# Performance work log

Hardware: AMD Instinct MI355X
Metric: run time of the kernel (lower is better)

## Reference

```python
import jax, jax.numpy as jnp
import numpy as np

TWO_PI = 2.0 * np.pi
EPS = 1e-12  # torch F.normalize eps


def setup_inputs() -> dict:
    key = jax.random.key(0)
    ks = jax.random.split(key, 12)
    B, NS, G = 16, 128, 20000
    P, S, E, T = 200, 128, 128, 50
    return {
        "x_genes": jax.random.normal(ks[0], (B, NS, G), jnp.float32),
        "tissue_idx": jax.random.randint(ks[1], (B, NS), 0, T, jnp.int32),
        "pathway_idx": jax.random.randint(ks[2], (P, S), 0, G, jnp.int32),
        "W_proj": jax.random.normal(ks[3], (P, E, S), jnp.float32) * (1.0 / np.sqrt(S)),
        "b_proj": jax.random.normal(ks[4], (P, E), jnp.float32) * 0.02,
        "tissue_table": jax.random.normal(ks[5], (T, E), jnp.float32),
        "W1": jax.random.normal(ks[6], (E, 32), jnp.float32) * (1.0 / np.sqrt(E)),
        "b1": jax.random.normal(ks[7], (32,), jnp.float32) * 0.02,
        "W2": jax.random.normal(ks[8], (32, 2), jnp.float32) * (1.0 / np.sqrt(32)),
        "b2": jax.random.normal(ks[9], (2,), jnp.float32) * 0.02,
        "Wdec": jax.random.normal(ks[10], (2, G), jnp.float32) * (1.0 / np.sqrt(2.0)),
        "bdec": jax.random.normal(ks[11], (G,), jnp.float32) * 0.02,
    }


def _l2norm(v):
    n = jnp.sqrt(jnp.sum(v * v, axis=-1, keepdims=True))
    return v / jnp.maximum(n, EPS)


def reference(x_genes, tissue_idx, pathway_idx, W_proj, b_proj, tissue_table,
              W1, b1, W2, b2, Wdec, bdec):
    B, NS, G = x_genes.shape
    x = x_genes.reshape(-1, G)            # [N, G], N = B*NS
    t = tissue_idx.reshape(-1)            # [N]

    # Pathway tokenizer: gather gene subsets + per-pathway linear (grouped GEMM)
    xg = x[:, pathway_idx]                # [N, P, S]
    H = jax.nn.relu(jnp.einsum('nps,pes->npe', xg, W_proj) + b_proj)  # [N, P, E]

    # Single-query attention with tissue embedding as query
    Q = tissue_table[t]                   # [N, E]
    scale = 1.0 / np.sqrt(H.shape[-1])
    scores = jnp.einsum('ne,npe->np', Q, H) * scale   # [N, P]
    attn = jax.nn.softmax(scores, axis=-1)
    context = jnp.einsum('np,npe->ne', attn, H)       # [N, E]

    # to_latent MLP (dropout=0 / eval)
    h = jax.nn.relu(context @ W1 + b1)
    pc = h @ W2 + b2                      # [N, 2]
    pcn = _l2norm(pc)
    ang = jnp.remainder(jnp.arctan2(pcn[:, 1], pcn[:, 0]) + TWO_PI, TWO_PI)

    # decode + normalize
    rec = _l2norm(pcn @ Wdec + bdec)      # [N, G]

    return (pcn.reshape(B, NS, 2), ang.reshape(B, NS), rec.reshape(B, NS, G))
```

## Files before the change

### kernel.cpp

```cpp
#include <hip/hip_runtime.h>
#include <cmath>

#define GG 20000
#define NN 2048
#define PP 200
#define SS 128
#define EE 128
#define TN 128
#define TPP 4
#define NSPLIT 50

typedef __bf16 bf16x8 __attribute__((ext_vector_type(8)));
typedef float f32x16 __attribute__((ext_vector_type(16)));
typedef unsigned short u16x8 __attribute__((ext_vector_type(8)));

__device__ __align__(16) unsigned g_xTi[(size_t)GG * NN];
__device__ __align__(16) unsigned short g_Wsw[(size_t)PP * 2 * 16384];
__device__ float g_ctx[(size_t)NN * NSPLIT * EE];
__device__ float g_m[NN * NSPLIT];
__device__ float g_l[NN * NSPLIT];
__device__ float g_pcn[NN * 2];

__device__ __forceinline__ unsigned short f2bf(float f) {
  unsigned u = __builtin_bit_cast(unsigned, f);
  return (unsigned short)((u + 0x7FFFu + ((u >> 16) & 1u)) >> 16);
}
__device__ __forceinline__ float bf2f(unsigned short h) {
  return __builtin_bit_cast(float, (unsigned)h << 16);
}
__device__ __forceinline__ unsigned packhl(float f) {
  unsigned short h = f2bf(f);
  unsigned short l = f2bf(f - bf2f(h));
  return (unsigned)h | ((unsigned)l << 16);
}

__global__ __launch_bounds__(256) void transpose_convert_kernel(
    const float* __restrict__ x)
{
  __shared__ float tile[64][65];
  const int g0 = blockIdx.x * 64;
  const int n0 = blockIdx.y * 64;
  const int t = threadIdx.x;
  {
    const int gq = t & 15, nl4 = t >> 4;
    #pragma unroll
    for (int k = 0; k < 4; ++k) {
      int nl = nl4 + 16 * k;
      int g = g0 + gq * 4;
      if (g + 3 < GG) {
        float4 v = *(const float4*)&x[(size_t)(n0 + nl) * GG + g];
        tile[gq * 4 + 0][nl] = v.x;
        tile[gq * 4 + 1][nl] = v.y;
        tile[gq * 4 + 2][nl] = v.z;
        tile[gq * 4 + 3][nl] = v.w;
      }
    }
  }
  __syncthreads();
  {
    const int nq = t & 15, gl4 = t >> 4;
    #pragma unroll
    for (int k = 0; k < 4; ++k) {
      int gl = gl4 + 16 * k;
      int g = g0 + gl;
      if (g < GG) {
        uint4 v;
        v.x = packhl(tile[gl][nq * 4 + 0]);
        v.y = packhl(tile[gl][nq * 4 + 1]);
        v.z = packhl(tile[gl][nq * 4 + 2]);
        v.w = packhl(tile[gl][nq * 4 + 3]);
        *(uint4*)&g_xTi[(size_t)g * NN + n0 + nq * 4] = v;
      }
    }
  }
}

__global__ __launch_bounds__(256) void wconvert_kernel(const float* __restrict__ Wp)
{
  unsigned v = blockIdx.x * 256 + threadIdx.x;
  const int si = v & 7;
  const int slp = (v >> 3) & 7;
  const int e = (v >> 6) & 127;
  const int ch = (v >> 13) & 1;
  const int p = v >> 14;
  const int slot = slp ^ (e & 7);
  const int s = ch * 64 + slot * 8 + si;
  float f = Wp[((size_t)p * EE + e) * SS + s];
  unsigned short h = f2bf(f);
  unsigned short l = f2bf(f - bf2f(h));
  size_t base = (size_t)(p * 2 + ch) * 16384 + e * 64 + slp * 8 + si;
  g_Wsw[base] = h;
  g_Wsw[base + 8192] = l;
}

__device__ __forceinline__ void stage_w(int p, int ch, unsigned short* ldsbase,
                                        int w, int ln) {
  const unsigned short* src = g_Wsw + (size_t)(p * 2 + ch) * 16384 + w * 4096 + ln * 8;
  unsigned short* ld = ldsbase + w * 4096;
  #pragma unroll
  for (int j = 0; j < 8; ++j) {
    __builtin_amdgcn_global_load_lds(
        (const __attribute__((address_space(1))) unsigned int*)(src + j * 512),
        (__attribute__((address_space(3))) unsigned int*)(ld + j * 512), 16, 0, 0);
  }
}

__device__ __forceinline__ void load_x(const int* __restrict__ pidx, int p, int ch,
                                       int kh, int ncol, unsigned* xr) {
  const int* pg = pidx + p * SS + ch * 64 + kh * 8;
  #pragma unroll
  for (int ks = 0; ks < 4; ++ks)
    #pragma unroll
    for (int j = 0; j < 8; ++j) {
      int g = pg[ks * 16 + j];
      xr[ks * 8 + j] = g_xTi[(size_t)g * NN + ncol];
    }
}

__device__ __forceinline__ void compute_chunk(const unsigned short* wb,
                                              const unsigned* xr, f32x16* acc,
                                              int nl, int kh) {
  const unsigned short* wAh = wb;
  const unsigned short* wAl = wb + 8192;
  #pragma unroll
  for (int ks = 0; ks < 4; ++ks) {
    u16x8 bhu, blu;
    #pragma unroll
    for (int j = 0; j < 8; ++j) {
      unsigned v = xr[ks * 8 + j];
      bhu[j] = (unsigned short)(v & 0xffffu);
      blu[j] = (unsigned short)(v >> 16);
    }
    bf16x8 bh = __builtin_bit_cast(bf16x8, bhu);
    bf16x8 bl = __builtin_bit_cast(bf16x8, blu);
    #pragma unroll
    for (int et = 0; et < 4; ++et) {
      const int e = et * 32 + nl;
      const int slp = (ks * 2 + kh) ^ (e & 7);
      bf16x8 ah = __builtin_bit_cast(bf16x8, *(const uint4*)(wAh + e * 64 + slp * 8));
      bf16x8 al = __builtin_bit_cast(bf16x8, *(const uint4*)(wAl + e * 64 + slp * 8));
      acc[et] = __builtin_amdgcn_mfma_f32_32x32x16_bf16(ah, bh, acc[et], 0, 0, 0);
      acc[et] = __builtin_amdgcn_mfma_f32_32x32x16_bf16(ah, bl, acc[et], 0, 0, 0);
      acc[et] = __builtin_amdgcn_mfma_f32_32x32x16_bf16(al, bh, acc[et], 0, 0, 0);
    }
  }
}

__global__ __launch_bounds__(256, 2) void proj_mfma_kernel(
    const int* __restrict__ tidx, const int* __restrict__ pidx,
    const float* __restrict__ bp, const float* __restrict__ tt)
{
  __shared__ __align__(16) unsigned short wbuf[2][16384];

  const int t = threadIdx.x;
  const int w = t >> 6;
  const int ln = t & 63;
  const int nl = ln & 31;
  const int kh = ln >> 5;
  const int n0 = blockIdx.x * TN;
  const int split = blockIdx.y;
  const int ncol = n0 + w * 32 + nl;
  const int tid_n = tidx[ncol];

  f32x16 ctx[4];
  #pragma unroll
  for (int et = 0; et < 4; ++et)
    #pragma unroll
    for (int r = 0; r < 16; ++r) ctx[et][r] = 0.f;
  float m_r = -1e30f, l_r = 0.f;

  unsigned xA[32], xB[32];

  {
    const int p = split * TPP;
    stage_w(p, 0, wbuf[0], w, ln);
    load_x(pidx, p, 0, kh, ncol, xA);
  }
  __syncthreads();

  for (int pp = 0; pp < TPP; ++pp) {
    const int p = split * TPP + pp;
    f32x16 acc[4];
    #pragma unroll
    for (int et = 0; et < 4; ++et)
      #pragma unroll
      for (int r = 0; r < 16; ++r) acc[et][r] = 0.f;

    stage_w(p, 1, wbuf[1], w, ln);
    load_x(pidx, p, 1, kh, ncol, xB);
    compute_chunk(wbuf[0], xA, acc, nl, kh);
    __syncthreads();

    if (pp + 1 < TPP) {
      stage_w(p + 1, 0, wbuf[0], w, ln);
      load_x(pidx, p + 1, 0, kh, ncol, xA);
    }
    compute_chunk(wbuf[1], xB, acc, nl, kh);

    const float4* qp = (const float4*)(tt + (size_t)tid_n * EE);
    const float4* bpv = (const float4*)(bp + (size_t)p * EE);
    float scr = 0.f;
    #pragma unroll
    for (int et = 0; et < 4; ++et)
      #pragma unroll
      for (int rq = 0; rq < 4; ++rq) {
        int e4 = (et * 32 + rq * 8 + kh * 4) >> 2;
        float4 q4 = qp[e4];
        float4 b4 = bpv[e4];
        float h0 = fmaxf(acc[et][rq * 4 + 0] + b4.x, 0.f);
        float h1 = fmaxf(acc[et][rq * 4 + 1] + b4.y, 0.f);
        float h2 = fmaxf(acc[et][rq * 4 + 2] + b4.z, 0.f);
        float h3 = fmaxf(acc[et][rq * 4 + 3] + b4.w, 0.f);
        acc[et][rq * 4 + 0] = h0; acc[et][rq * 4 + 1] = h1;
        acc[et][rq * 4 + 2] = h2; acc[et][rq * 4 + 3] = h3;
        scr += h0 * q4.x + h1 * q4.y + h2 * q4.z + h3 * q4.w;
      }
    scr += __shfl_xor(scr, 32);
    const float s_r = scr * 0.08838834764831845f;
    const float mn = fmaxf(m_r, s_r);
    const float f = expf(m_r - mn);
    const float wg = expf(s_r - mn);
    l_r = l_r * f + wg;
    m_r = mn;
    #pragma unroll
    for (int et = 0; et < 4; ++et)
      #pragma unroll
      for (int r = 0; r < 16; ++r)
        ctx[et][r] = ctx[et][r] * f + wg * acc[et][r];

    __syncthreads();
  }

  float* tbuf = (float*)wbuf;
  float* tb = tbuf + w * (32 * 128);
  #pragma unroll
  for (int et = 0; et < 4; ++et)
    #pragma unroll
    for (int rq = 0; rq < 4; ++rq) {
      int slot = et * 8 + rq * 2 + kh;
      float4 v = make_float4(ctx[et][rq * 4 + 0], ctx[et][rq * 4 + 1],
                             ctx[et][rq * 4 + 2], ctx[et][rq * 4 + 3]);
      *(float4*)&tb[nl * 128 + ((slot ^ nl) << 2)] = v;
    }
  __syncthreads();
  {
    const int rrow = ln >> 1, eh = (ln & 1) * 16;
    const int nn = n0 + w * 32 + rrow;
    float* dst = g_ctx + ((size_t)nn * NSPLIT + split) * EE + eh * 4;
    const float* srcrow = tb + rrow * 128;
    #pragma unroll
    for (int k = 0; k < 16; ++k) {
      int slot = eh + k;
      *(float4*)&dst[k * 4] = *(const float4*)&srcrow[(slot ^ rrow) << 2];
    }
  }
  if (ln < 32) {
    g_m[(size_t)ncol * NSPLIT + split] = m_r;
    g_l[(size_t)ncol * NSPLIT + split] = l_r;
  }
}

__global__ __launch_bounds__(128) void combine_kernel(
    const float* __restrict__ W1, const float* __restrict__ b1,
    const float* __restrict__ W2, const float* __restrict__ b2,
    float* __restrict__ out)
{
  const int n = blockIdx.x;
  const int t = threadIdx.x;
  __shared__ float sm[NSPLIT], slv[NSPLIT], ws[NSPLIT], ctxs[EE], hsh[32];

  if (t < NSPLIT) sm[t] = g_m[(size_t)n * NSPLIT + t];
  else if (t < 2 * NSPLIT) slv[t - NSPLIT] = g_l[(size_t)n * NSPLIT + t - NSPLIT];
  __syncthreads();
  if (t < NSPLIT) {
    float M = -1e30f;
    for (int s = 0; s < NSPLIT; ++s) M = fmaxf(M, sm[s]);
    ws[t] = expf(sm[t] - M);
  }
  __syncthreads();
  float L = 0.f;
  for (int s = 0; s < NSPLIT; ++s) L += slv[s] * ws[s];
  float c = 0.f;
  for (int s = 0; s < NSPLIT; ++s)
    c += ws[s] * g_ctx[((size_t)n * NSPLIT + s) * EE + t];
  ctxs[t] = c / L;
  __syncthreads();
  if (t < 32) {
    float h = b1[t];
    for (int e = 0; e < EE; ++e) h += ctxs[e] * W1[e * 32 + t];
    hsh[t] = fmaxf(h, 0.f);
  }
  __syncthreads();
  if (t == 0) {
    float p0 = b2[0], p1 = b2[1];
    #pragma unroll
    for (int k = 0; k < 32; ++k) { p0 += hsh[k] * W2[k * 2]; p1 += hsh[k] * W2[k * 2 + 1]; }
    float inv = 1.f / fmaxf(sqrtf(p0 * p0 + p1 * p1), 1e-12f);
    float q0 = p0 * inv, q1 = p1 * inv;
    const float PI2 = 6.2831853071795864769f;
    float ang = atan2f(q1, q0) + PI2;
    if (ang >= PI2) ang -= PI2;
    out[n * 2 + 0] = q0;
    out[n * 2 + 1] = q1;
    out[2 * NN + n] = ang;
    g_pcn[n * 2 + 0] = q0;
    g_pcn[n * 2 + 1] = q1;
  }
}

__global__ __launch_bounds__(256) void rec_kernel(
    const float* __restrict__ Wdec, const float* __restrict__ bdec,
    float* __restrict__ out)
{
  const int n = blockIdx.x;
  const int t = threadIdx.x;
  __shared__ float red[4];

  const float q0 = g_pcn[n * 2 + 0];
  const float q1 = g_pcn[n * 2 + 1];

  float ss = 0.f;
  for (int i = t; i < GG / 4; i += 256) {
    float4 w0 = *(const float4*)&Wdec[i * 4];
    float4 w1 = *(const float4*)&Wdec[GG + i * 4];
    float4 bd = *(const float4*)&bdec[i * 4];
    float v0 = q0 * w0.x + q1 * w1.x + bd.x;
    float v1 = q0 * w0.y + q1 * w1.y + bd.y;
    float v2 = q0 * w0.z + q1 * w1.z + bd.z;
    float v3 = q0 * w0.w + q1 * w1.w + bd.w;
    ss += v0 * v0 + v1 * v1 + v2 * v2 + v3 * v3;
  }
  #pragma unroll
  for (int off = 32; off >= 1; off >>= 1) ss += __shfl_xor(ss, off);
  if ((t & 63) == 0) red[t >> 6] = ss;
  __syncthreads();
  const float inv = 1.f / fmaxf(sqrtf(red[0] + red[1] + red[2] + red[3]), 1e-12f);

  float* orec = out + 3 * NN + (size_t)n * GG;
  for (int i = t; i < GG / 4; i += 256) {
    float4 w0 = *(const float4*)&Wdec[i * 4];
    float4 w1 = *(const float4*)&Wdec[GG + i * 4];
    float4 bd = *(const float4*)&bdec[i * 4];
    float4 o;
    o.x = (q0 * w0.x + q1 * w1.x + bd.x) * inv;
    o.y = (q0 * w0.y + q1 * w1.y + bd.y) * inv;
    o.z = (q0 * w0.z + q1 * w1.z + bd.z) * inv;
    o.w = (q0 * w0.w + q1 * w1.w + bd.w) * inv;
    *(float4*)&orec[i * 4] = o;
  }
}

extern "C" void kernel_launch(void* const* d_in, const int* in_sizes, int n_in,
                              void* d_out, int out_size, void* d_ws, size_t ws_size,
                              hipStream_t stream) {
  (void)in_sizes; (void)n_in; (void)out_size; (void)d_ws; (void)ws_size;
  const float* x    = (const float*)d_in[0];
  const int*   tidx = (const int*)  d_in[1];
  const int*   pidx = (const int*)  d_in[2];
  const float* Wp   = (const float*)d_in[3];
  const float* bp   = (const float*)d_in[4];
  const float* tt   = (const float*)d_in[5];
  const float* W1   = (const float*)d_in[6];
  const float* b1   = (const float*)d_in[7];
  const float* W2   = (const float*)d_in[8];
  const float* b2   = (const float*)d_in[9];
  const float* Wdec = (const float*)d_in[10];
  const float* bdec = (const float*)d_in[11];
  float* out = (float*)d_out;

  dim3 gridT((GG + 63) / 64, NN / 64, 1);
  transpose_convert_kernel<<<gridT, 256, 0, stream>>>(x);
  wconvert_kernel<<<(PP * 16384) / 256, 256, 0, stream>>>(Wp);

  dim3 gridA(NN / TN, NSPLIT, 1);
  proj_mfma_kernel<<<gridA, 256, 0, stream>>>(tidx, pidx, bp, tt);

  combine_kernel<<<NN, 128, 0, stream>>>(W1, b1, W2, b2, out);
  rec_kernel<<<NN, 256, 0, stream>>>(Wdec, bdec, out);
}
```

Before: 348.0 us.

## Assign one pathway per block and move the softmax reduction into combine

The projection kernel drops the per-block loop over 4 pathways and its double-buffered online softmax. Each block now handles a single pathway: it loads that pathway's full weights into LDS at once and writes the raw score and ReLU output per pathway. The combine kernel then computes the softmax over all 200 pathway scores with warp reductions and takes the weighted sum of the contexts using 256 threads. This creates more blocks and shorter dependency chains, but the per-pathway context buffer grows fourfold, so global write and read traffic rises sharply, and load/compute overlap is lost.

```diff
diff --git a/kernel.cpp b/kernel.cpp
--- a/kernel.cpp
+++ b/kernel.cpp
@@ -7,18 +7,16 @@
 #define SS 128
 #define EE 128
 #define TN 128
-#define TPP 4
-#define NSPLIT 50
+#define NSPLIT 200
 
 typedef __bf16 bf16x8 __attribute__((ext_vector_type(8)));
 typedef float f32x16 __attribute__((ext_vector_type(16)));
 typedef unsigned short u16x8 __attribute__((ext_vector_type(8)));
 
 __device__ __align__(16) unsigned g_xTi[(size_t)GG * NN];
-__device__ __align__(16) unsigned short g_Wsw[(size_t)PP * 2 * 16384];
+__device__ __align__(16) unsigned short g_Wsw[(size_t)PP * 32768];
 __device__ float g_ctx[(size_t)NN * NSPLIT * EE];
 __device__ float g_m[NN * NSPLIT];
-__device__ float g_l[NN * NSPLIT];
 __device__ float g_pcn[NN * 2];
 
 __device__ __forceinline__ unsigned short f2bf(float f) {
@@ -93,64 +91,13 @@
   g_Wsw[base + 8192] = l;
 }
 
-__device__ __forceinline__ void stage_w(int p, int ch, unsigned short* ldsbase,
-                                        int w, int ln) {
-  const unsigned short* src = g_Wsw + (size_t)(p * 2 + ch) * 16384 + w * 4096 + ln * 8;
-  unsigned short* ld = ldsbase + w * 4096;
-  #pragma unroll
-  for (int j = 0; j < 8; ++j) {
-    __builtin_amdgcn_global_load_lds(
-        (const __attribute__((address_space(1))) unsigned int*)(src + j * 512),
-        (__attribute__((address_space(3))) unsigned int*)(ld + j * 512), 16, 0, 0);
-  }
-}
-
-__device__ __forceinline__ void load_x(const int* __restrict__ pidx, int p, int ch,
-                                       int kh, int ncol, unsigned* xr) {
-  const int* pg = pidx + p * SS + ch * 64 + kh * 8;
-  #pragma unroll
-  for (int ks = 0; ks < 4; ++ks)
-    #pragma unroll
-    for (int j = 0; j < 8; ++j) {
-      int g = pg[ks * 16 + j];
-      xr[ks * 8 + j] = g_xTi[(size_t)g * NN + ncol];
-    }
-}
-
-__device__ __forceinline__ void compute_chunk(const unsigned short* wb,
-                                              const unsigned* xr, f32x16* acc,
-                                              int nl, int kh) {
-  const unsigned short* wAh = wb;
-  const unsigned short* wAl = wb + 8192;
-  #pragma unroll
-  for (int ks = 0; ks < 4; ++ks) {
-    u16x8 bhu, blu;
-    #pragma unroll
-    for (int j = 0; j < 8; ++j) {
-      unsigned v = xr[ks * 8 + j];
-      bhu[j] = (unsigned short)(v & 0xffffu);
-      blu[j] = (unsigned short)(v >> 16);
-    }
-    bf16x8 bh = __builtin_bit_cast(bf16x8, bhu);
-    bf16x8 bl = __builtin_bit_cast(bf16x8, blu);
-    #pragma unroll
-    for (int et = 0; et < 4; ++et) {
-      const int e = et * 32 + nl;
-      const int slp = (ks * 2 + kh) ^ (e & 7);
-      bf16x8 ah = __builtin_bit_cast(bf16x8, *(const uint4*)(wAh + e * 64 + slp * 8));
-      bf16x8 al = __builtin_bit_cast(bf16x8, *(const uint4*)(wAl + e * 64 + slp * 8));
-      acc[et] = __builtin_amdgcn_mfma_f32_32x32x16_bf16(ah, bh, acc[et], 0, 0, 0);
-      acc[et] = __builtin_amdgcn_mfma_f32_32x32x16_bf16(ah, bl, acc[et], 0, 0, 0);
-      acc[et] = __builtin_amdgcn_mfma_f32_32x32x16_bf16(al, bh, acc[et], 0, 0, 0);
-    }
-  }
-}
-
 __global__ __launch_bounds__(256, 2) void proj_mfma_kernel(
     const int* __restrict__ tidx, const int* __restrict__ pidx,
     const float* __restrict__ bp, const float* __restrict__ tt)
 {
-  __shared__ __align__(16) unsigned short wbuf[2][16384];
+  __shared__ __align__(16) unsigned short wbuf[32768];
+  __shared__ int sidx[SS];
+  __shared__ float sbp[EE];
 
   const int t = threadIdx.x;
   const int w = t >> 6;
@@ -158,95 +105,104 @@
   const int nl = ln & 31;
   const int kh = ln >> 5;
   const int n0 = blockIdx.x * TN;
-  const int split = blockIdx.y;
+  const int p = blockIdx.y;
   const int ncol = n0 + w * 32 + nl;
   const int tid_n = tidx[ncol];
 
-  f32x16 ctx[4];
+  if (t < 128) sidx[t] = pidx[p * SS + t];
+  else         sbp[t - 128] = bp[p * EE + (t - 128)];
+  __syncthreads();
+
+  {
+    const unsigned short* src = g_Wsw + (size_t)p * 32768 + w * 512 + ln * 8;
+    unsigned short* dst = wbuf + w * 512;
+    #pragma unroll
+    for (int j = 0; j < 16; ++j) {
+      __builtin_amdgcn_global_load_lds(
+          (const __attribute__((address_space(1))) unsigned int*)(src + j * 2048),
+          (__attribute__((address_space(3))) unsigned int*)(dst + j * 2048), 16, 0, 0);
+    }
+  }
+
+  unsigned xr[64];
+  #pragma unroll
+  for (int ks = 0; ks < 8; ++ks)
+    #pragma unroll
+    for (int j = 0; j < 8; ++j) {
+      int s = ks * 16 + kh * 8 + j;
+      int g = sidx[s];
+      xr[ks * 8 + j] = g_xTi[(size_t)g * NN + ncol];
+    }
+  __syncthreads();
+
+  f32x16 acc[4];
   #pragma unroll
   for (int et = 0; et < 4; ++et)
     #pragma unroll
-    for (int r = 0; r < 16; ++r) ctx[et][r] = 0.f;
-  float m_r = -1e30f, l_r = 0.f;
-
-  unsigned xA[32], xB[32];
-
-  {
-    const int p = split * TPP;
-    stage_w(p, 0, wbuf[0], w, ln);
-    load_x(pidx, p, 0, kh, ncol, xA);
-  }
-  __syncthreads();
-
-  for (int pp = 0; pp < TPP; ++pp) {
-    const int p = split * TPP + pp;
-    f32x16 acc[4];
-    #pragma unroll
-    for (int et = 0; et < 4; ++et)
-      #pragma unroll
-      for (int r = 0; r < 16; ++r) acc[et][r] = 0.f;
-
-    stage_w(p, 1, wbuf[1], w, ln);
-    load_x(pidx, p, 1, kh, ncol, xB);
-    compute_chunk(wbuf[0], xA, acc, nl, kh);
-    __syncthreads();
-
-    if (pp + 1 < TPP) {
-      stage_w(p + 1, 0, wbuf[0], w, ln);
-      load_x(pidx, p + 1, 0, kh, ncol, xA);
-    }
-    compute_chunk(wbuf[1], xB, acc, nl, kh);
-
-    const float4* qp = (const float4*)(tt + (size_t)tid_n * EE);
-    const float4* bpv = (const float4*)(bp + (size_t)p * EE);
-    float scr = 0.f;
-    #pragma unroll
-    for (int et = 0; et < 4; ++et)
-      #pragma unroll
-      for (int rq = 0; rq < 4; ++rq) {
-        int e4 = (et * 32 + rq * 8 + kh * 4) >> 2;
-        float4 q4 = qp[e4];
-        float4 b4 = bpv[e4];
-        float h0 = fmaxf(acc[et][rq * 4 + 0] + b4.x, 0.f);
-        float h1 = fmaxf(acc[et][rq * 4 + 1] + b4.y, 0.f);
-        float h2 = fmaxf(acc[et][rq * 4 + 2] + b4.z, 0.f);
-        float h3 = fmaxf(acc[et][rq * 4 + 3] + b4.w, 0.f);
-        acc[et][rq * 4 + 0] = h0; acc[et][rq * 4 + 1] = h1;
-        acc[et][rq * 4 + 2] = h2; acc[et][rq * 4 + 3] = h3;
-        scr += h0 * q4.x + h1 * q4.y + h2 * q4.z + h3 * q4.w;
-      }
-    scr += __shfl_xor(scr, 32);
-    const float s_r = scr * 0.08838834764831845f;
-    const float mn = fmaxf(m_r, s_r);
-    const float f = expf(m_r - mn);
-    const float wg = expf(s_r - mn);
-    l_r = l_r * f + wg;
-    m_r = mn;
-    #pragma unroll
-    for (int et = 0; et < 4; ++et)
-      #pragma unroll
-      for (int r = 0; r < 16; ++r)
-        ctx[et][r] = ctx[et][r] * f + wg * acc[et][r];
-
-    __syncthreads();
-  }
-
-  float* tbuf = (float*)wbuf;
-  float* tb = tbuf + w * (32 * 128);
+    for (int r = 0; r < 16; ++r) acc[et][r] = 0.f;
+
+  #pragma unroll
+  for (int ks = 0; ks < 8; ++ks) {
+    const unsigned short* wAh = wbuf + (ks >> 2) * 16384;
+    const unsigned short* wAl = wAh + 8192;
+    const int ksl = ks & 3;
+    u16x8 bhu, blu;
+    #pragma unroll
+    for (int j = 0; j < 8; ++j) {
+      unsigned v = xr[ks * 8 + j];
+      bhu[j] = (unsigned short)(v & 0xffffu);
+      blu[j] = (unsigned short)(v >> 16);
+    }
+    bf16x8 bh = __builtin_bit_cast(bf16x8, bhu);
+    bf16x8 bl = __builtin_bit_cast(bf16x8, blu);
+    #pragma unroll
+    for (int et = 0; et < 4; ++et) {
+      const int e = et * 32 + nl;
+      const int slp = (ksl * 2 + kh) ^ (e & 7);
+      bf16x8 ah = __builtin_bit_cast(bf16x8, *(const uint4*)(wAh + e * 64 + slp * 8));
+      bf16x8 al = __builtin_bit_cast(bf16x8, *(const uint4*)(wAl + e * 64 + slp * 8));
+      acc[et] = __builtin_amdgcn_mfma_f32_32x32x16_bf16(ah, bh, acc[et], 0, 0, 0);
+      acc[et] = __builtin_amdgcn_mfma_f32_32x32x16_bf16(ah, bl, acc[et], 0, 0, 0);
+      acc[et] = __builtin_amdgcn_mfma_f32_32x32x16_bf16(al, bh, acc[et], 0, 0, 0);
+    }
+  }
+
+  const float4* qp = (const float4*)(tt + (size_t)tid_n * EE);
+  float scr = 0.f;
+  #pragma unroll
+  for (int et = 0; et < 4; ++et)
+    #pragma unroll
+    for (int rq = 0; rq < 4; ++rq) {
+      int e4 = (et * 32 + rq * 8 + kh * 4) >> 2;
+      float4 q4 = qp[e4];
+      float4 b4 = *(const float4*)&sbp[e4 * 4];
+      float h0 = fmaxf(acc[et][rq * 4 + 0] + b4.x, 0.f);
+      float h1 = fmaxf(acc[et][rq * 4 + 1] + b4.y, 0.f);
+      float h2 = fmaxf(acc[et][rq * 4 + 2] + b4.z, 0.f);
+      float h3 = fmaxf(acc[et][rq * 4 + 3] + b4.w, 0.f);
+      acc[et][rq * 4 + 0] = h0; acc[et][rq * 4 + 1] = h1;
+      acc[et][rq * 4 + 2] = h2; acc[et][rq * 4 + 3] = h3;
+      scr += h0 * q4.x + h1 * q4.y + h2 * q4.z + h3 * q4.w;
+    }
+  scr += __shfl_xor(scr, 32);
+  const float s_r = scr * 0.08838834764831845f;
+
+  __syncthreads();
+  float* tb = ((float*)wbuf) + w * (32 * 128);
   #pragma unroll
   for (int et = 0; et < 4; ++et)
     #pragma unroll
     for (int rq = 0; rq < 4; ++rq) {
       int slot = et * 8 + rq * 2 + kh;
-      float4 v = make_float4(ctx[et][rq * 4 + 0], ctx[et][rq * 4 + 1],
-                             ctx[et][rq * 4 + 2], ctx[et][rq * 4 + 3]);
+      float4 v = make_float4(acc[et][rq * 4 + 0], acc[et][rq * 4 + 1],
+                             acc[et][rq * 4 + 2], acc[et][rq * 4 + 3]);
       *(float4*)&tb[nl * 128 + ((slot ^ nl) << 2)] = v;
     }
   __syncthreads();
   {
     const int rrow = ln >> 1, eh = (ln & 1) * 16;
     const int nn = n0 + w * 32 + rrow;
-    float* dst = g_ctx + ((size_t)nn * NSPLIT + split) * EE + eh * 4;
+    float* dst = g_ctx + ((size_t)nn * NSPLIT + p) * EE + eh * 4;
     const float* srcrow = tb + rrow * 128;
     #pragma unroll
     for (int k = 0; k < 16; ++k) {
@@ -254,41 +210,51 @@
       *(float4*)&dst[k * 4] = *(const float4*)&srcrow[(slot ^ rrow) << 2];
     }
   }
-  if (ln < 32) {
-    g_m[(size_t)ncol * NSPLIT + split] = m_r;
-    g_l[(size_t)ncol * NSPLIT + split] = l_r;
-  }
-}
-
-__global__ __launch_bounds__(128) void combine_kernel(
+  if (ln < 32) g_m[(size_t)ncol * NSPLIT + p] = s_r;
+}
+
+__global__ __launch_bounds__(256) void combine_kernel(
     const float* __restrict__ W1, const float* __restrict__ b1,
     const float* __restrict__ W2, const float* __restrict__ b2,
     float* __restrict__ out)
 {
   const int n = blockIdx.x;
   const int t = threadIdx.x;
-  __shared__ float sm[NSPLIT], slv[NSPLIT], ws[NSPLIT], ctxs[EE], hsh[32];
-
-  if (t < NSPLIT) sm[t] = g_m[(size_t)n * NSPLIT + t];
-  else if (t < 2 * NSPLIT) slv[t - NSPLIT] = g_l[(size_t)n * NSPLIT + t - NSPLIT];
-  __syncthreads();
-  if (t < NSPLIT) {
-    float M = -1e30f;
-    for (int s = 0; s < NSPLIT; ++s) M = fmaxf(M, sm[s]);
-    ws[t] = expf(sm[t] - M);
-  }
-  __syncthreads();
-  float L = 0.f;
-  for (int s = 0; s < NSPLIT; ++s) L += slv[s] * ws[s];
-  float c = 0.f;
-  for (int s = 0; s < NSPLIT; ++s)
-    c += ws[s] * g_ctx[((size_t)n * NSPLIT + s) * EE + t];
-  ctxs[t] = c / L;
-  __syncthreads();
+  __shared__ float ws[NSPLIT];
+  __shared__ float ctx2[2][EE];
+  __shared__ float r1[4], r2[4];
+  __shared__ float hsh[32];
+
+  float mv = (t < NSPLIT) ? g_m[(size_t)n * NSPLIT + t] : -1e30f;
+  float M = mv;
+  #pragma unroll
+  for (int off = 32; off >= 1; off >>= 1) M = fmaxf(M, __shfl_xor(M, off));
+  if ((t & 63) == 0) r1[t >> 6] = M;
+  __syncthreads();
+  M = fmaxf(fmaxf(r1[0], r1[1]), fmaxf(r1[2], r1[3]));
+  float wv = (t < NSPLIT) ? expf(mv - M) : 0.f;
+  if (t < NSPLIT) ws[t] = wv;
+  float L = wv;
+  #pragma unroll
+  for (int off = 32; off >= 1; off >>= 1) L += __shfl_xor(L, off);
+  if ((t & 63) == 0) r2[t >> 6] = L;
+  __syncthreads();
+  L = r2[0] + r2[1] + r2[2] + r2[3];
+
+  {
+    const int e = t & 127, hf = t >> 7;
+    const float* base = g_ctx + ((size_t)n * NSPLIT + hf * 100) * EE + e;
+    float c = 0.f;
+    #pragma unroll 4
+    for (int s = 0; s < 100; ++s) c += ws[hf * 100 + s] * base[(size_t)s * EE];
+    ctx2[hf][e] = c;
+  }
+  __syncthreads();
+  const float invL = 1.f / L;
   if (t < 32) {
-    float h = b1[t];
-    for (int e = 0; e < EE; ++e) h += ctxs[e] * W1[e * 32 + t];
-    hsh[t] = fmaxf(h, 0.f);
+    float h = 0.f;
+    for (int e = 0; e < EE; ++e) h += (ctx2[0][e] + ctx2[1][e]) * W1[e * 32 + t];
+    hsh[t] = fmaxf(h * invL + b1[t], 0.f);
   }
   __syncthreads();
   if (t == 0) {
@@ -375,6 +341,6 @@
   dim3 gridA(NN / TN, NSPLIT, 1);
   proj_mfma_kernel<<<gridA, 256, 0, stream>>>(tidx, pidx, bp, tt);
 
-  combine_kernel<<<NN, 128, 0, stream>>>(W1, b1, W2, b2, out);
+  combine_kernel<<<NN, 256, 0, stream>>>(W1, b1, W2, b2, out);
   rec_kernel<<<NN, 256, 0, stream>>>(Wdec, bdec, out);
 }
```

Measured after the change: 363.0 us. +4.3%, slower.
